# Kernel tuning notes

Hardware: AMD Instinct MI355X
Metric: run time of the kernel (lower is better)

## Reference

```python
import jax, jax.numpy as jnp
import numpy as np

N, E, C, MID = 20000, 320000, 16, 32
EPS = 1e-8

# ---- real Clebsch-Gordan (Q_J) matrices for degree pairs up to l=1, real-SH m-order (-l..l) i.e. (y,z,x) for l=1 ----

def _q_matrices():
    Q0 = np.eye(3, dtype=np.float32)[:, :, None] / np.sqrt(3.0)          # 1x1 -> J=0
    eps = np.zeros((3, 3, 3), dtype=np.float32)
    for (a, b, c_) in [(0, 1, 2), (1, 2, 0), (2, 0, 1)]:
        eps[a, b, c_] = 1.0
        eps[a, c_, b] = -1.0
    Q1 = eps / np.sqrt(2.0)                                               # 1x1 -> J=1 (cross product)
    Q2 = np.zeros((3, 3, 5), dtype=np.float32)                            # 1x1 -> J=2 (sym traceless)
    s2 = 1.0 / np.sqrt(2.0); s6 = 1.0 / np.sqrt(6.0)
    Q2[2, 0, 0] = Q2[0, 2, 0] = s2          # ~xy
    Q2[0, 1, 1] = Q2[1, 0, 1] = s2          # ~yz
    Q2[0, 0, 2] = -s6; Q2[1, 1, 2] = 2 * s6; Q2[2, 2, 2] = -s6  # ~(2z2-x2-y2)
    Q2[1, 2, 3] = Q2[2, 1, 3] = s2          # ~xz
    Q2[2, 2, 4] = s2; Q2[0, 0, 4] = -s2     # ~(x2-y2)
    return Q0, Q1, Q2

_Q0, _Q1, _Q2 = _q_matrices()


def _basis(u):
    """u: [E,3] unit edge directions -> basis tensors per (d_in,d_out) pair."""
    x, y, z = u[:, 0], u[:, 1], u[:, 2]
    Ep = u.shape[0]
    Y0 = jnp.full((Ep,), 0.28209479177387814, u.dtype)
    Y1 = 0.4886025119029199 * jnp.stack([y, z, x], -1)                    # m=-1,0,1
    Y2 = jnp.stack([1.0925484305920792 * x * y,
                    1.0925484305920792 * y * z,
                    0.31539156525252005 * (3.0 * z * z - 1.0),
                    1.0925484305920792 * x * z,
                    0.5462742152960396 * (x * x - y * y)], -1)
    b00 = Y0.reshape(Ep, 1, 1, 1, 1, 1)
    b01 = Y1.reshape(Ep, 1, 3, 1, 1, 1)
    b10 = Y1.reshape(Ep, 1, 1, 1, 3, 1)
    K0 = Y0[:, None, None] * jnp.asarray(_Q0[:, :, 0])
    K1 = jnp.einsum('em,abm->eab', Y1, jnp.asarray(_Q1))
    K2 = jnp.einsum('em,abm->eab', Y2, jnp.asarray(_Q2))
    b11 = jnp.stack([K0, K1, K2], -1).reshape(Ep, 1, 3, 1, 3, 3)          # num_freq=3 (J=0,1,2)
    return b00, b01, b10, b11


def _bn(x, g, b):  # BatchNorm1d, training-mode stats over edges, eps=1e-5
    mu = x.mean(0)
    var = ((x - mu) ** 2).mean(0)
    return (x - mu) * jax.lax.rsqrt(var + 1e-5) * g + b


def _hidden(feat, W1, b1, g1, be1, W2, b2, g2, be2):
    h = jax.nn.relu(_bn(feat @ W1 + b1, g1, be1))
    return jax.nn.relu(_bn(h @ W2 + b2, g2, be2))


def _kernel(Rflat, basis, nco, do_dim, nci, di_dim, nf):
    # RadialFunc output view: [E, nc_out, 1, nc_in, 1, num_freq]; contract freq with basis
    R = Rflat.reshape(-1, nco, 1, nci, 1, nf)
    k = (R * basis).sum(-1)                        # [E,nco,do_dim,nci,di_dim]
    return k.reshape(-1, nco * do_dim, nci * di_dim)


def _norm_bias(x, bias):  # GNormBias: relu(|x| + b) * phase
    n = jnp.sqrt((x * x).sum(-1, keepdims=True) + 1e-12)
    phase = x / jnp.maximum(n, EPS)
    return jax.nn.relu(n[..., 0] + bias)[..., None] * phase


def _forward(src, dst, pos, c, v, w,
             rW1, rb1, rg1, rbe1, rW2, rb2, rg2, rbe2,
             w3_a00, b3_a00, w3_a01, b3_a01, w3_a10, b3_a10, w3_a11, b3_a11,
             w3_b01, b3_b01, w3_b11, b3_b11,
             selfA0, selfA1, selfB1, nbias0, nbias1):
    n_nodes = c.shape[0]
    n_edges = src.shape[0]
    rel = pos[dst] - pos[src]
    r = jnp.sqrt((rel * rel).sum(-1, keepdims=True))                      # [E,1]
    u = rel / jnp.maximum(r, EPS)
    b00, b01, b10, b11 = _basis(u)
    feat = jnp.concatenate([w, r], -1)                                    # [E, edge_dim+1]
    # all 6 radial-net hiddens at once: [6,E,MID]
    H = jax.vmap(_hidden, in_axes=(None, 0, 0, 0, 0, 0, 0, 0, 0))(
        feat, rW1, rb1, rg1, rbe1, rW2, rb2, rg2, rbe2)
    deg = jax.ops.segment_sum(jnp.ones((n_edges,), feat.dtype), dst, num_segments=n_nodes)
    inv = (1.0 / jnp.maximum(deg, 1.0))[:, None, None]
    mask = (deg > 0).astype(feat.dtype)[:, None, None]
    # ---- layer A: in {0:1,1:1} -> mid {0:C,1:C} ----
    k00 = _kernel(H[0] @ w3_a00 + b3_a00, b00, C, 1, 1, 1, 1)             # [E,C,1]
    k01 = _kernel(H[1] @ w3_a01 + b3_a01, b01, C, 3, 1, 1, 1)             # [E,3C,1]
    k10 = _kernel(H[2] @ w3_a10 + b3_a10, b10, C, 1, 1, 3, 1)             # [E,C,3]
    k11 = _kernel(H[3] @ w3_a11 + b3_a11, b11, C, 3, 1, 3, 3)             # [E,3C,3]
    s0 = c[src].reshape(n_edges, 1, 1)
    s1 = v[src].reshape(n_edges, 3, 1)
    m0 = (k00 @ s0 + k10 @ s1).reshape(n_edges, C, 1)
    m1 = (k01 @ s0 + k11 @ s1).reshape(n_edges, C, 3)
    h0 = jax.ops.segment_sum(m0, dst, num_segments=n_nodes) * inv \
         + jnp.einsum('oi,nid->nod', selfA0[0], c) * mask
    h1 = jax.ops.segment_sum(m1, dst, num_segments=n_nodes) * inv \
         + jnp.einsum('oi,nid->nod', selfA1[0], v) * mask
    # ---- GNormBias on mid fiber ----
    h0 = _norm_bias(h0, nbias0)
    h1 = _norm_bias(h1, nbias1)
    # ---- layer B: mid {0:C,1:C} -> out {1:2} ----
    kb01 = _kernel(H[4] @ w3_b01 + b3_b01, b01, 2, 3, C, 1, 1)            # [E,6,C]
    kb11 = _kernel(H[5] @ w3_b11 + b3_b11, b11, 2, 3, C, 3, 3)            # [E,6,3C]
    t0 = h0[src]                                                          # [E,C,1]
    t1 = h1[src].reshape(n_edges, C * 3, 1)
    mB = (kb01 @ t0 + kb11 @ t1).reshape(n_edges, 2, 3)
    out = jax.ops.segment_sum(mB, dst, num_segments=n_nodes) * inv \
          + jnp.einsum('oi,nid->nod', selfB1[0], h1) * mask
    return out                                                            # [N,2,3]


def setup_inputs() -> dict:
    key = jax.random.key(0)
    ks = jax.random.split(key, 40)
    def rn(i, shape, scale=1.0):
        return jax.random.normal(ks[i], shape, jnp.float32) * scale
    K = 6
    sc = 1.0 / np.sqrt(MID)
    d = {}
    d['src'] = jax.random.randint(ks[0], (E,), 0, N)
    d['dst'] = jax.random.randint(ks[1], (E,), 0, N)
    d['pos'] = rn(2, (N, 3))
    d['c'] = rn(3, (N, 1, 1))
    d['v'] = rn(4, (N, 1, 3))
    d['w'] = rn(5, (E, 1))
    d['rW1'] = rn(6, (K, 2, MID), 1.0 / np.sqrt(2.0))
    d['rb1'] = jnp.zeros((K, MID), jnp.float32)
    d['rg1'] = jnp.ones((K, MID), jnp.float32)
    d['rbe1'] = jnp.zeros((K, MID), jnp.float32)
    d['rW2'] = rn(7, (K, MID, MID), sc)
    d['rb2'] = jnp.zeros((K, MID), jnp.float32)
    d['rg2'] = jnp.ones((K, MID), jnp.float32)
    d['rbe2'] = jnp.zeros((K, MID), jnp.float32)
    d['w3_a00'] = rn(8, (MID, C), sc);      d['b3_a00'] = jnp.zeros((C,), jnp.float32)
    d['w3_a01'] = rn(9, (MID, C), sc);      d['b3_a01'] = jnp.zeros((C,), jnp.float32)
    d['w3_a10'] = rn(10, (MID, C), sc);     d['b3_a10'] = jnp.zeros((C,), jnp.float32)
    d['w3_a11'] = rn(11, (MID, 3 * C), sc); d['b3_a11'] = jnp.zeros((3 * C,), jnp.float32)
    d['w3_b01'] = rn(12, (MID, 2 * C), sc); d['b3_b01'] = jnp.zeros((2 * C,), jnp.float32)
    d['w3_b11'] = rn(13, (MID, 6 * C), sc); d['b3_b11'] = jnp.zeros((6 * C,), jnp.float32)
    d['selfA0'] = rn(14, (1, C, 1))
    d['selfA1'] = rn(15, (1, C, 1))
    d['selfB1'] = rn(16, (1, 2, C), 1.0 / np.sqrt(C))
    d['nbias0'] = rn(17, (C,))
    d['nbias1'] = rn(18, (C,))
    return d


def reference(src, dst, pos, c, v, w,
              rW1, rb1, rg1, rbe1, rW2, rb2, rg2, rbe2,
              w3_a00, b3_a00, w3_a01, b3_a01, w3_a10, b3_a10, w3_a11, b3_a11,
              w3_b01, b3_b01, w3_b11, b3_b11,
              selfA0, selfA1, selfB1, nbias0, nbias1):
    return _forward(src, dst, pos, c, v, w,
                    rW1, rb1, rg1, rbe1, rW2, rb2, rg2, rbe2,
                    w3_a00, b3_a00, w3_a01, b3_a01, w3_a10, b3_a10, w3_a11, b3_a11,
                    w3_b01, b3_b01, w3_b11, b3_b11,
                    selfA0, selfA1, selfB1, nbias0, nbias1)
```

## Files before the change

### kernel.cpp

```cpp
#include <hip/hip_runtime.h>

#define NN 20000
#define NE 320000
#define CDIM 16
#define MID 32
#define EPSF 1e-8f

#define SCHED_FENCE() __builtin_amdgcn_sched_barrier(0)

#define OFF_DEGI   848
#define ZERO_WORDS 20848
#define OFF_ROWPTR 20848
#define OFF_CURSOR 40864
#define OFF_EORDER 60864
#define OFF_SRCS   380864
#define OFF_WSRT   700864
#define OFF_FW1A   1020864
#define OFF_FW1B   1021056
#define OFF_FC1    1021248
#define OFF_BN2A   1021440
#define OFF_FC2    1021632
#define OFF_FW2T   1021824
#define OFF_ECS    1027968
#define OFF_H0N    2307968
#define OFF_H1N    2627968
#define OFF_MSGA0  3587968
#define OFF_MSGA1  8707968
#define OFF_MSGB   24067968

#define Y0C   0.28209479177387814f
#define Y1C   0.4886025119029199f
#define Y2C1  1.0925484305920792f
#define Y2C2  0.31539156525252005f
#define Y2C3  0.5462742152960396f
#define S2C   0.7071067811865476f
#define S6C   0.4082482904638631f
#define K0C   0.16286750396763996f

__device__ __forceinline__ void atomAddD(double* p, double v) {
  unsafeAtomicAdd(p, v);
}

__device__ __forceinline__ void mlpH_lds(
    const float* __restrict__ a1, const float* __restrict__ b1v,
    const float* __restrict__ c1, const float* __restrict__ c2,
    const float* __restrict__ W2T, float we, float r, float* H) {
  float h[MID];
#pragma unroll
  for (int j4 = 0; j4 < 8; ++j4) {
    float4 av = ((const float4*)a1)[j4];
    float4 bv = ((const float4*)b1v)[j4];
    float4 cv = ((const float4*)c1)[j4];
    h[4 * j4 + 0] = fmaxf(fmaf(we, av.x, fmaf(r, bv.x, cv.x)), 0.0f);
    h[4 * j4 + 1] = fmaxf(fmaf(we, av.y, fmaf(r, bv.y, cv.y)), 0.0f);
    h[4 * j4 + 2] = fmaxf(fmaf(we, av.z, fmaf(r, bv.z, cv.z)), 0.0f);
    h[4 * j4 + 3] = fmaxf(fmaf(we, av.w, fmaf(r, bv.w, cv.w)), 0.0f);
  }
  SCHED_FENCE();
#pragma unroll
  for (int jg = 0; jg < 8; ++jg) {
#pragma unroll
    for (int jq = 0; jq < 4; ++jq) {
      const int j = jg * 4 + jq;
      float acc = c2[j];
      const float4* wp = (const float4*)(W2T + j * MID);
#pragma unroll
      for (int i4 = 0; i4 < 8; ++i4) {
        float4 wv = wp[i4];
        acc = fmaf(h[4 * i4 + 0], wv.x, acc);
        acc = fmaf(h[4 * i4 + 1], wv.y, acc);
        acc = fmaf(h[4 * i4 + 2], wv.z, acc);
        acc = fmaf(h[4 * i4 + 3], wv.w, acc);
      }
      H[j] = fmaxf(acc, 0.0f);
    }
    SCHED_FENCE();
  }
}

__global__ __launch_bounds__(256) void k_hist(
    const int* __restrict__ dst, float* __restrict__ ws) {
  int e = blockIdx.x * blockDim.x + threadIdx.x;
  if (e >= NE) return;
  atomicAdd((int*)ws + OFF_DEGI + dst[e], 1);
}

__global__ void k_scan(float* __restrict__ ws) {
  __shared__ int buf[256];
  __shared__ int carry;
  const int* degi = (const int*)ws + OFF_DEGI;
  int* rowptr = (int*)ws + OFF_ROWPTR;
  int* cursor = (int*)ws + OFF_CURSOR;
  int tid = threadIdx.x;
  if (tid == 0) carry = 0;
  __syncthreads();
  for (int base = 0; base < NN; base += 256) {
    int v = (base + tid < NN) ? degi[base + tid] : 0;
    buf[tid] = v;
    __syncthreads();
    for (int off = 1; off < 256; off <<= 1) {
      int t = buf[tid];
      int add = (tid >= off) ? buf[tid - off] : 0;
      __syncthreads();
      buf[tid] = t + add;
      __syncthreads();
    }
    int excl = buf[tid] - v;
    if (base + tid < NN) {
      rowptr[base + tid] = carry + excl;
      cursor[base + tid] = carry + excl;
    }
    __syncthreads();
    if (tid == 255) carry += buf[255];
    __syncthreads();
  }
  if (tid == 0) rowptr[NN] = carry;
}

__global__ __launch_bounds__(256) void k_scatter(
    const int* __restrict__ dst, float* __restrict__ ws) {
  int e = blockIdx.x * blockDim.x + threadIdx.x;
  if (e >= NE) return;
  int* cursor = (int*)ws + OFF_CURSOR;
  int* eorder = (int*)ws + OFF_EORDER;
  int d = dst[e];
  int p = atomicAdd(cursor + d, 1);
  eorder[p] = e;
}

__global__ __launch_bounds__(256) void k_geo(
    const int* __restrict__ src, const int* __restrict__ dst,
    const float* __restrict__ pos, const float* __restrict__ w,
    float* __restrict__ ws) {
  __shared__ double sred[20];
  double lw = 0, lr = 0, lww = 0, lrr = 0, lwr = 0;
  const int* eorder = (const int*)ws + OFF_EORDER;
  int* srcs = (int*)ws + OFF_SRCS;
  float* wsrt = ws + OFF_WSRT;
  float4* ecs = (float4*)(ws + OFF_ECS);
  for (int t = blockIdx.x * blockDim.x + threadIdx.x; t < NE;
       t += gridDim.x * blockDim.x) {
    int e = eorder[t];
    int s = src[e], d = dst[e];
    float dx = pos[3 * d + 0] - pos[3 * s + 0];
    float dy = pos[3 * d + 1] - pos[3 * s + 1];
    float dz = pos[3 * d + 2] - pos[3 * s + 2];
    float r = sqrtf(dx * dx + dy * dy + dz * dz);
    float ri = 1.0f / fmaxf(r, EPSF);
    ecs[t] = make_float4(r, dx * ri, dy * ri, dz * ri);
    float we = w[e];
    wsrt[t] = we;
    srcs[t] = s;
    double wd = (double)we, rd = (double)r;
    lw += wd; lr += rd; lww += wd * wd; lrr += rd * rd; lwr += wd * rd;
  }
#pragma unroll
  for (int d = 32; d >= 1; d >>= 1) {
    lw += __shfl_xor(lw, d);
    lr += __shfl_xor(lr, d);
    lww += __shfl_xor(lww, d);
    lrr += __shfl_xor(lrr, d);
    lwr += __shfl_xor(lwr, d);
  }
  int wid = threadIdx.x >> 6;
  if ((threadIdx.x & 63) == 0) {
    sred[0 * 4 + wid] = lw;
    sred[1 * 4 + wid] = lr;
    sred[2 * 4 + wid] = lww;
    sred[3 * 4 + wid] = lrr;
    sred[4 * 4 + wid] = lwr;
  }
  __syncthreads();
  if (threadIdx.x < 5) {
    double v = sred[threadIdx.x * 4 + 0] + sred[threadIdx.x * 4 + 1]
             + sred[threadIdx.x * 4 + 2] + sred[threadIdx.x * 4 + 3];
    atomAddD((double*)ws + threadIdx.x * 8, v);
  }
}

__global__ void k_fin1(const float* __restrict__ rW1, const float* __restrict__ rb1,
                       const float* __restrict__ rg1, const float* __restrict__ rbe1,
                       float* __restrict__ ws) {
  int t = threadIdx.x;
  int k = t >> 5, j = t & 31;
  const double* s1 = (const double*)ws;
  double Sw = s1[0], Sr = s1[8], Sww = s1[16], Srr = s1[24], Swr = s1[32];
  const double inv = 1.0 / (double)NE;
  double W0 = (double)rW1[k * 64 + j], W1 = (double)rW1[k * 64 + 32 + j];
  double b = (double)rb1[k * 32 + j];
  double mlin = (Sw * W0 + Sr * W1) * inv;
  double mu = mlin + b;
  double ex2 = (Sww * W0 * W0 + Srr * W1 * W1 + 2.0 * Swr * W0 * W1) * inv
             + 2.0 * b * mlin + b * b;
  double var = ex2 - mu * mu;
  double a = (double)rg1[k * 32 + j] / sqrt(var + 1e-5);
  ws[OFF_FW1A + t] = (float)(W0 * a);
  ws[OFF_FW1B + t] = (float)(W1 * a);
  ws[OFF_FC1 + t] = (float)((double)rbe1[k * 32 + j] - mlin * a);
}

__global__ __launch_bounds__(256) void k_stats2(
    const float* __restrict__ rW2, const float* __restrict__ rb2,
    float* __restrict__ ws) {
  const int k = blockIdx.y;
  const int j0 = blockIdx.z * 16;
  __shared__ __align__(16) float sW1a[32], sW1b[32], sc1[32];
  __shared__ __align__(16) float sW2c[512];
  __shared__ float sb2[16];
  __shared__ float sredf[2][16][4];
  int tid = threadIdx.x;
  if (tid < 32) {
    sW1a[tid] = ws[OFF_FW1A + k * 32 + tid];
    sW1b[tid] = ws[OFF_FW1B + k * 32 + tid];
    sc1[tid] = ws[OFF_FC1 + k * 32 + tid];
  }
  if (tid < 16) sb2[tid] = rb2[k * 32 + j0 + tid];
  for (int t = tid; t < 512; t += 256) {
    int jj = t >> 5, i = t & 31;
    sW2c[t] = rW2[k * 1024 + i * 32 + j0 + jj];
  }
  __syncthreads();
  const float4* ecs = (const float4*)(ws + OFF_ECS);
  const float* wsrt = ws + OFF_WSRT;
  float lsum[16], lsq[16];
#pragma unroll
  for (int jj = 0; jj < 16; ++jj) { lsum[jj] = 0.0f; lsq[jj] = 0.0f; }
  const int NP = NE / 2;
  for (int p = blockIdx.x * blockDim.x + tid; p < NP;
       p += gridDim.x * blockDim.x) {
    int e0 = 2 * p;
    float r0 = ecs[e0].x, r1 = ecs[e0 + 1].x;
    float w0 = wsrt[e0], w1 = wsrt[e0 + 1];
    float h0[MID], h1[MID];
#pragma unroll
    for (int j4 = 0; j4 < 8; ++j4) {
      float4 av = ((const float4*)sW1a)[j4];
      float4 bv = ((const float4*)sW1b)[j4];
      float4 cv = ((const float4*)sc1)[j4];
      h0[4 * j4 + 0] = fmaxf(fmaf(w0, av.x, fmaf(r0, bv.x, cv.x)), 0.0f);
      h1[4 * j4 + 0] = fmaxf(fmaf(w1, av.x, fmaf(r1, bv.x, cv.x)), 0.0f);
      h0[4 * j4 + 1] = fmaxf(fmaf(w0, av.y, fmaf(r0, bv.y, cv.y)), 0.0f);
      h1[4 * j4 + 1] = fmaxf(fmaf(w1, av.y, fmaf(r1, bv.y, cv.y)), 0.0f);
      h0[4 * j4 + 2] = fmaxf(fmaf(w0, av.z, fmaf(r0, bv.z, cv.z)), 0.0f);
      h1[4 * j4 + 2] = fmaxf(fmaf(w1, av.z, fmaf(r1, bv.z, cv.z)), 0.0f);
      h0[4 * j4 + 3] = fmaxf(fmaf(w0, av.w, fmaf(r0, bv.w, cv.w)), 0.0f);
      h1[4 * j4 + 3] = fmaxf(fmaf(w1, av.w, fmaf(r1, bv.w, cv.w)), 0.0f);
    }
    SCHED_FENCE();
#pragma unroll
    for (int jg = 0; jg < 4; ++jg) {
#pragma unroll
      for (int jq = 0; jq < 4; ++jq) {
        const int jj = jg * 4 + jq;
        float aE0 = sb2[jj], aE1 = sb2[jj];
        const float4* wp = (const float4*)(sW2c + jj * 32);
#pragma unroll
        for (int i4 = 0; i4 < 8; ++i4) {
          float4 wv = wp[i4];
          aE0 = fmaf(h0[4 * i4 + 0], wv.x, aE0);
          aE1 = fmaf(h1[4 * i4 + 0], wv.x, aE1);
          aE0 = fmaf(h0[4 * i4 + 1], wv.y, aE0);
          aE1 = fmaf(h1[4 * i4 + 1], wv.y, aE1);
          aE0 = fmaf(h0[4 * i4 + 2], wv.z, aE0);
          aE1 = fmaf(h1[4 * i4 + 2], wv.z, aE1);
          aE0 = fmaf(h0[4 * i4 + 3], wv.w, aE0);
          aE1 = fmaf(h1[4 * i4 + 3], wv.w, aE1);
        }
        lsum[jj] += aE0 + aE1;
        lsq[jj] = fmaf(aE0, aE0, fmaf(aE1, aE1, lsq[jj]));
      }
      SCHED_FENCE();
    }
  }
  int wid = tid >> 6;
#pragma unroll
  for (int jj = 0; jj < 16; ++jj) {
    float v1 = lsum[jj], v2 = lsq[jj];
#pragma unroll
    for (int d = 32; d >= 1; d >>= 1) {
      v1 += __shfl_xor(v1, d);
      v2 += __shfl_xor(v2, d);
    }
    if ((tid & 63) == 0) {
      sredf[0][jj][wid] = v1;
      sredf[1][jj][wid] = v2;
    }
  }
  __syncthreads();
  if (tid < 32) {
    int jj = tid & 15, which = tid >> 4;
    float v = sredf[which][jj][0] + sredf[which][jj][1]
            + sredf[which][jj][2] + sredf[which][jj][3];
    double* s2 = (double*)(ws + 80);
    atomAddD(s2 + k * 64 + which * 32 + j0 + jj, (double)v);
  }
}

__global__ void k_fin2(const float* __restrict__ rb2,
                       const float* __restrict__ rg2, const float* __restrict__ rbe2,
                       float* __restrict__ ws) {
  int t = threadIdx.x;
  int k = t >> 5, j = t & 31;
  const double* s2 = (const double*)(ws + 80);
  const double inv = 1.0 / (double)NE;
  double mu = s2[k * 64 + j] * inv;
  double ex2 = s2[k * 64 + 32 + j] * inv;
  double var = ex2 - mu * mu;
  double a = (double)rg2[t] / sqrt(var + 1e-5);
  ws[OFF_BN2A + t] = (float)a;
  ws[OFF_FC2 + t] = (float)((double)rbe2[t] + ((double)rb2[t] - mu) * a);
}

__global__ __launch_bounds__(256) void k_fold2(const float* __restrict__ rW2,
                                               float* __restrict__ ws) {
  int idx = blockIdx.x * blockDim.x + threadIdx.x;
  if (idx >= 6144) return;
  int k = idx >> 10, rem = idx & 1023;
  int j = rem >> 5, i = rem & 31;
  ws[OFF_FW2T + idx] = rW2[k * 1024 + i * 32 + j] * ws[OFF_BN2A + k * 32 + j];
}

__global__ __launch_bounds__(256) void k_passA0(
    const float* __restrict__ cI, const float* __restrict__ vI,
    const float* __restrict__ w00, const float* __restrict__ b00,
    const float* __restrict__ w10, const float* __restrict__ b10,
    float* __restrict__ ws) {
  __shared__ __align__(16) float sW1a[64], sW1b[64], sc1[64], sc2[64];
  __shared__ __align__(16) float sW2T[2048];
  __shared__ __align__(16) float sP00[512], sP10[512];
  __shared__ float sB00[16], sB10[16];
  int tid = threadIdx.x;
  if (tid < 32) {
    sW1a[tid] = ws[OFF_FW1A + tid];       sW1a[32 + tid] = ws[OFF_FW1A + 64 + tid];
    sW1b[tid] = ws[OFF_FW1B + tid];       sW1b[32 + tid] = ws[OFF_FW1B + 64 + tid];
    sc1[tid]  = ws[OFF_FC1 + tid];        sc1[32 + tid]  = ws[OFF_FC1 + 64 + tid];
    sc2[tid]  = ws[OFF_FC2 + tid];        sc2[32 + tid]  = ws[OFF_FC2 + 64 + tid];
  }
  for (int t = tid; t < 1024; t += 256) {
    sW2T[t] = ws[OFF_FW2T + t];
    sW2T[1024 + t] = ws[OFF_FW2T + 2048 + t];
  }
  for (int t = tid; t < 512; t += 256) {
    int i = t >> 4, co = t & 15;
    sP00[co * 32 + i] = w00[t];
    sP10[co * 32 + i] = w10[t];
  }
  if (tid < 16) { sB00[tid] = b00[tid]; sB10[tid] = b10[tid]; }
  __syncthreads();

  const int* srcs = (const int*)ws + OFF_SRCS;
  const float* wsrt = ws + OFF_WSRT;
  const float4* ecs = (const float4*)(ws + OFF_ECS);
  int t = blockIdx.x * blockDim.x + tid;
  if (t >= NE) return;
  int s = srcs[t];
  float4 E = ecs[t];
  float we = wsrt[t];
  float cs = cI[s];
  float v0 = vI[3 * s + 0], v1 = vI[3 * s + 1], v2 = vI[3 * s + 2];
  float dY1v = Y1C * (E.z * v0 + E.w * v1 + E.y * v2);

  float H[MID], m0[CDIM];
  mlpH_lds(sW1a, sW1b, sc1, sc2, sW2T, we, E.x, H);
  float f0 = Y0C * cs;
#pragma unroll
  for (int cg = 0; cg < 4; ++cg) {
#pragma unroll
    for (int cq = 0; cq < 4; ++cq) {
      const int co = cg * 4 + cq;
      float a = sB00[co];
      const float4* wp = (const float4*)(sP00 + co * 32);
#pragma unroll
      for (int i4 = 0; i4 < 8; ++i4) {
        float4 wv = wp[i4];
        a = fmaf(H[4 * i4 + 0], wv.x, a);
        a = fmaf(H[4 * i4 + 1], wv.y, a);
        a = fmaf(H[4 * i4 + 2], wv.z, a);
        a = fmaf(H[4 * i4 + 3], wv.w, a);
      }
      m0[co] = a * f0;
    }
    SCHED_FENCE();
  }
  mlpH_lds(sW1a + 32, sW1b + 32, sc1 + 32, sc2 + 32, sW2T + 1024, we, E.x, H);
#pragma unroll
  for (int cg = 0; cg < 4; ++cg) {
#pragma unroll
    for (int cq = 0; cq < 4; ++cq) {
      const int co = cg * 4 + cq;
      float a = sB10[co];
      const float4* wp = (const float4*)(sP10 + co * 32);
#pragma unroll
      for (int i4 = 0; i4 < 8; ++i4) {
        float4 wv = wp[i4];
        a = fmaf(H[4 * i4 + 0], wv.x, a);
        a = fmaf(H[4 * i4 + 1], wv.y, a);
        a = fmaf(H[4 * i4 + 2], wv.z, a);
        a = fmaf(H[4 * i4 + 3], wv.w, a);
      }
      m0[co] = fmaf(a, dY1v, m0[co]);
    }
    SCHED_FENCE();
  }
  float4* mp = (float4*)(ws + OFF_MSGA0) + t * 4;
#pragma unroll
  for (int q = 0; q < 4; ++q)
    mp[q] = make_float4(m0[4 * q], m0[4 * q + 1], m0[4 * q + 2], m0[4 * q + 3]);
}

__global__ __launch_bounds__(256) void k_passA1(
    const float* __restrict__ cI, const float* __restrict__ vI,
    const float* __restrict__ w01, const float* __restrict__ b01,
    const float* __restrict__ w11, const float* __restrict__ b11,
    float* __restrict__ ws) {
  __shared__ __align__(16) float sW1a[64], sW1b[64], sc1[64], sc2[64];
  __shared__ __align__(16) float sW2T[2048];
  __shared__ __align__(16) float sP01[512], sP11[1536];
  __shared__ float sB01[16], sB11[48];
  int tid = threadIdx.x;
  if (tid < 32) {
    sW1a[tid] = ws[OFF_FW1A + 32 + tid];  sW1a[32 + tid] = ws[OFF_FW1A + 96 + tid];
    sW1b[tid] = ws[OFF_FW1B + 32 + tid];  sW1b[32 + tid] = ws[OFF_FW1B + 96 + tid];
    sc1[tid]  = ws[OFF_FC1 + 32 + tid];   sc1[32 + tid]  = ws[OFF_FC1 + 96 + tid];
    sc2[tid]  = ws[OFF_FC2 + 32 + tid];   sc2[32 + tid]  = ws[OFF_FC2 + 96 + tid];
  }
  for (int t = tid; t < 1024; t += 256) {
    sW2T[t] = ws[OFF_FW2T + 1024 + t];
    sW2T[1024 + t] = ws[OFF_FW2T + 3072 + t];
  }
  for (int t = tid; t < 512; t += 256) {
    int i = t >> 4, co = t & 15;
    sP01[co * 32 + i] = w01[t];
  }
  for (int t = tid; t < 1536; t += 256) {
    int i = t / 48, c = t - i * 48;
    sP11[c * 32 + i] = w11[t];
  }
  if (tid < 16) sB01[tid] = b01[tid];
  if (tid < 48) sB11[tid] = b11[tid];
  __syncthreads();

  const int* srcs = (const int*)ws + OFF_SRCS;
  const float* wsrt = ws + OFF_WSRT;
  const float4* ecs = (const float4*)(ws + OFF_ECS);
  int t = blockIdx.x * blockDim.x + tid;
  if (t >= NE) return;
  int s = srcs[t];
  float4 E = ecs[t];
  float we = wsrt[t];
  float cs = cI[s];

  float H[MID];
  float ra[16];
  mlpH_lds(sW1a, sW1b, sc1, sc2, sW2T, we, E.x, H);
#pragma unroll
  for (int cg = 0; cg < 4; ++cg) {
#pragma unroll
    for (int cq = 0; cq < 4; ++cq) {
      const int co = cg * 4 + cq;
      float a = sB01[co];
      const float4* wp = (const float4*)(sP01 + co * 32);
#pragma unroll
      for (int i4 = 0; i4 < 8; ++i4) {
        float4 wv = wp[i4];
        a = fmaf(H[4 * i4 + 0], wv.x, a);
        a = fmaf(H[4 * i4 + 1], wv.y, a);
        a = fmaf(H[4 * i4 + 2], wv.z, a);
        a = fmaf(H[4 * i4 + 3], wv.w, a);
      }
      ra[co] = a;
    }
    SCHED_FENCE();
  }
  mlpH_lds(sW1a + 32, sW1b + 32, sc1 + 32, sc2 + 32, sW2T + 1024, we, E.x, H);
  float y10 = Y1C * E.z, y11 = Y1C * E.w, y12 = Y1C * E.y;
  float KV[3][3];
  {
    float ux = E.y, uy = E.z, uz = E.w;
    float y20 = Y2C1 * ux * uy, y21 = Y2C1 * uy * uz;
    float y22 = Y2C2 * (3.0f * uz * uz - 1.0f);
    float y23 = Y2C1 * ux * uz, y24 = Y2C3 * (ux * ux - uy * uy);
    float S00 = -S6C * y22 - S2C * y24;
    float S11 = 2.0f * S6C * y22;
    float S22 = -S6C * y22 + S2C * y24;
    float S01 = S2C * y21, S02 = S2C * y20, S12 = S2C * y23;
    float v0 = vI[3 * s + 0], v1 = vI[3 * s + 1], v2 = vI[3 * s + 2];
    KV[0][0] = K0C * v0; KV[0][1] = K0C * v1; KV[0][2] = K0C * v2;
    KV[1][0] = S2C * (y12 * v1 - y11 * v2);
    KV[1][1] = S2C * (y10 * v2 - y12 * v0);
    KV[1][2] = S2C * (y11 * v0 - y10 * v1);
    KV[2][0] = S00 * v0 + S01 * v1 + S02 * v2;
    KV[2][1] = S01 * v0 + S11 * v1 + S12 * v2;
    KV[2][2] = S02 * v0 + S12 * v1 + S22 * v2;
  }
  float cy0 = cs * y10, cy1 = cs * y11, cy2 = cs * y12;
#pragma unroll 1
  for (int g = 0; g < 4; ++g) {
    float a[12];
#pragma unroll
    for (int q = 0; q < 4; ++q) {
      int co = g * 4 + q;
      float R0 = sB11[co * 3 + 0], R1 = sB11[co * 3 + 1], R2 = sB11[co * 3 + 2];
      const float4* p0 = (const float4*)(sP11 + (co * 3 + 0) * 32);
      const float4* p1 = (const float4*)(sP11 + (co * 3 + 1) * 32);
      const float4* p2 = (const float4*)(sP11 + (co * 3 + 2) * 32);
#pragma unroll
      for (int i4 = 0; i4 < 8; ++i4) {
        float4 w0v = p0[i4], w1v = p1[i4], w2v = p2[i4];
        float h0 = H[4 * i4 + 0], h1 = H[4 * i4 + 1];
        float h2 = H[4 * i4 + 2], h3 = H[4 * i4 + 3];
        R0 = fmaf(h0, w0v.x, R0); R1 = fmaf(h0, w1v.x, R1); R2 = fmaf(h0, w2v.x, R2);
        R0 = fmaf(h1, w0v.y, R0); R1 = fmaf(h1, w1v.y, R1); R2 = fmaf(h1, w2v.y, R2);
        R0 = fmaf(h2, w0v.z, R0); R1 = fmaf(h2, w1v.z, R1); R2 = fmaf(h2, w2v.z, R2);
        R0 = fmaf(h3, w0v.w, R0); R1 = fmaf(h3, w1v.w, R1); R2 = fmaf(h3, w2v.w, R2);
      }
      float r_ = ra[co];
      a[q * 3 + 0] = fmaf(r_, cy0, R0 * KV[0][0] + R1 * KV[1][0] + R2 * KV[2][0]);
      a[q * 3 + 1] = fmaf(r_, cy1, R0 * KV[0][1] + R1 * KV[1][1] + R2 * KV[2][1]);
      a[q * 3 + 2] = fmaf(r_, cy2, R0 * KV[0][2] + R1 * KV[1][2] + R2 * KV[2][2]);
    }
    float4* mp = (float4*)(ws + OFF_MSGA1 + g * (NE * 12)) + t * 3;
    mp[0] = make_float4(a[0], a[1], a[2], a[3]);
    mp[1] = make_float4(a[4], a[5], a[6], a[7]);
    mp[2] = make_float4(a[8], a[9], a[10], a[11]);
    SCHED_FENCE();
  }
}

__global__ __launch_bounds__(256) void k_nodeA(
    const float* __restrict__ cI, const float* __restrict__ vI,
    const float* __restrict__ selfA0, const float* __restrict__ selfA1,
    const float* __restrict__ nbias0, const float* __restrict__ nbias1,
    float* __restrict__ ws) {
  int idx = blockIdx.x * blockDim.x + threadIdx.x;
  if (idx >= NN * CDIM) return;
  int n = idx >> 4, co = idx & 15;
  const int* rowptr = (const int*)ws + OFF_ROWPTR;
  int r0 = rowptr[n], r1 = rowptr[n + 1];
  const float* mA0 = ws + OFF_MSGA0;
  const float* mA1 = ws + OFF_MSGA1 + (co >> 2) * (NE * 12) + (co & 3) * 3;
  float x0 = 0.0f, xa = 0.0f, xb = 0.0f, xc = 0.0f;
  for (int row = r0; row < r1; ++row) {
    x0 += mA0[row * 16 + co];
    xa += mA1[row * 12 + 0];
    xb += mA1[row * 12 + 1];
    xc += mA1[row * 12 + 2];
  }
  float dg = (float)(r1 - r0);
  float iv = 1.0f / fmaxf(dg, 1.0f);
  float mk = dg > 0.0f ? 1.0f : 0.0f;
  x0 = x0 * iv + selfA0[co] * cI[n] * mk;
  float n0 = sqrtf(x0 * x0 + 1e-12f);
  ws[OFF_H0N + idx] = fmaxf(n0 + nbias0[co], 0.0f) * (x0 / fmaxf(n0, EPSF));
  xa = xa * iv + selfA1[co] * vI[3 * n + 0] * mk;
  xb = xb * iv + selfA1[co] * vI[3 * n + 1] * mk;
  xc = xc * iv + selfA1[co] * vI[3 * n + 2] * mk;
  float nv = sqrtf(xa * xa + xb * xb + xc * xc + 1e-12f);
  float sc = fmaxf(nv + nbias1[co], 0.0f) / fmaxf(nv, EPSF);
  ws[OFF_H1N + idx * 3 + 0] = xa * sc;
  ws[OFF_H1N + idx * 3 + 1] = xb * sc;
  ws[OFF_H1N + idx * 3 + 2] = xc * sc;
}

__global__ __launch_bounds__(256) void k_passB(
    const float* __restrict__ wb01, const float* __restrict__ bb01,
    const float* __restrict__ wb11, const float* __restrict__ bb11,
    float* __restrict__ ws) {
  __shared__ __align__(16) float sW1a[64], sW1b[64], sc1[64], sc2[64];
  __shared__ __align__(16) float sW2T[2048];
  __shared__ __align__(16) float sPB01[1024];
  __shared__ __align__(16) float sPB11[3072];
  __shared__ float sBB01[32];
  __shared__ float sBB11[96];
  int tid = threadIdx.x;
  if (tid < 64) {
    sW1a[tid] = ws[OFF_FW1A + 128 + tid];
    sW1b[tid] = ws[OFF_FW1B + 128 + tid];
    sc1[tid] = ws[OFF_FC1 + 128 + tid];
    sc2[tid] = ws[OFF_FC2 + 128 + tid];
  }
  for (int t = tid; t < 2048; t += 256) sW2T[t] = ws[OFF_FW2T + 4096 + t];
  for (int t = tid; t < 1024; t += 256) {
    int i = t >> 5, c = t & 31;
    int o = c >> 4, ci = c & 15;
    sPB01[(ci * 2 + o) * 32 + i] = wb01[t];
  }
  for (int t = tid; t < 3072; t += 256) {
    int i = t / 96, c = t - i * 96;
    int o = c / 48, rem = c - o * 48;
    int ci = rem / 3, f = rem - ci * 3;
    sPB11[(ci * 6 + o * 3 + f) * 32 + i] = wb11[t];
  }
  if (tid < 32) {
    int o = tid >> 4, ci = tid & 15;
    sBB01[ci * 2 + o] = bb01[tid];
  }
  if (tid < 96) {
    int o = tid / 48, rem = tid - o * 48;
    int ci = rem / 3, f = rem - ci * 3;
    sBB11[ci * 6 + o * 3 + f] = bb11[tid];
  }
  __syncthreads();

  const int* srcs = (const int*)ws + OFF_SRCS;
  const float* wsrt = ws + OFF_WSRT;
  const float4* ecs = (const float4*)(ws + OFF_ECS);
  int t = blockIdx.x * blockDim.x + tid;
  if (t >= NE) return;
  int s = srcs[t];
  float4 E = ecs[t];
  float we = wsrt[t];

  float H[MID];
  mlpH_lds(sW1a, sW1b, sc1, sc2, sW2T, we, E.x, H);
  const float* h0p = ws + OFF_H0N + s * CDIM;
  float A0 = 0.0f, A1 = 0.0f;
#pragma unroll 1
  for (int ci = 0; ci < CDIM; ++ci) {
    float b = h0p[ci];
    float R0 = sBB01[ci * 2 + 0], R1 = sBB01[ci * 2 + 1];
    const float4* p0 = (const float4*)(sPB01 + (ci * 2 + 0) * 32);
    const float4* p1 = (const float4*)(sPB01 + (ci * 2 + 1) * 32);
#pragma unroll
    for (int i4 = 0; i4 < 8; ++i4) {
      float4 w0v = p0[i4], w1v = p1[i4];
      float h0 = H[4 * i4 + 0], h1 = H[4 * i4 + 1];
      float h2 = H[4 * i4 + 2], h3 = H[4 * i4 + 3];
      R0 = fmaf(h0, w0v.x, R0); R1 = fmaf(h0, w1v.x, R1);
      R0 = fmaf(h1, w0v.y, R0); R1 = fmaf(h1, w1v.y, R1);
      R0 = fmaf(h2, w0v.z, R0); R1 = fmaf(h2, w1v.z, R1);
      R0 = fmaf(h3, w0v.w, R0); R1 = fmaf(h3, w1v.w, R1);
    }
    A0 = fmaf(R0, b, A0);
    A1 = fmaf(R1, b, A1);
    SCHED_FENCE();
  }
  mlpH_lds(sW1a + 32, sW1b + 32, sc1 + 32, sc2 + 32, sW2T + 1024, we, E.x, H);
  const float* h1p = ws + OFF_H1N + s * CDIM * 3;
  float G[6][3];
#pragma unroll
  for (int of = 0; of < 6; ++of) {
    G[of][0] = 0.0f; G[of][1] = 0.0f; G[of][2] = 0.0f;
  }
#pragma unroll 1
  for (int ci = 0; ci < CDIM; ++ci) {
    float b0 = h1p[ci * 3 + 0], b1 = h1p[ci * 3 + 1], b2 = h1p[ci * 3 + 2];
#pragma unroll
    for (int of = 0; of < 6; ++of) {
      float R = sBB11[ci * 6 + of];
      const float4* wp = (const float4*)(sPB11 + (ci * 6 + of) * 32);
#pragma unroll
      for (int i4 = 0; i4 < 8; ++i4) {
        float4 wv = wp[i4];
        R = fmaf(H[4 * i4 + 0], wv.x, R);
        R = fmaf(H[4 * i4 + 1], wv.y, R);
        R = fmaf(H[4 * i4 + 2], wv.z, R);
        R = fmaf(H[4 * i4 + 3], wv.w, R);
      }
      G[of][0] = fmaf(R, b0, G[of][0]);
      G[of][1] = fmaf(R, b1, G[of][1]);
      G[of][2] = fmaf(R, b2, G[of][2]);
    }
    SCHED_FENCE();
  }
  {
    float ux = E.y, uy = E.z, uz = E.w;
    float y10 = Y1C * uy, y11 = Y1C * uz, y12 = Y1C * ux;
    float y20 = Y2C1 * ux * uy, y21 = Y2C1 * uy * uz;
    float y22 = Y2C2 * (3.0f * uz * uz - 1.0f);
    float y23 = Y2C1 * ux * uz, y24 = Y2C3 * (ux * ux - uy * uy);
    float S00 = -S6C * y22 - S2C * y24;
    float S11 = 2.0f * S6C * y22;
    float S22 = -S6C * y22 + S2C * y24;
    float S01 = S2C * y21, S02 = S2C * y20, S12 = S2C * y23;
    float4* mp = (float4*)(ws + OFF_MSGB) + t * 2;
#pragma unroll
    for (int o = 0; o < 2; ++o) {
      float Ao = (o == 0) ? A0 : A1;
      float m0 = Ao * y10 + K0C * G[o * 3 + 0][0]
               + S2C * (y12 * G[o * 3 + 1][1] - y11 * G[o * 3 + 1][2])
               + S00 * G[o * 3 + 2][0] + S01 * G[o * 3 + 2][1] + S02 * G[o * 3 + 2][2];
      float m1 = Ao * y11 + K0C * G[o * 3 + 0][1]
               + S2C * (y10 * G[o * 3 + 1][2] - y12 * G[o * 3 + 1][0])
               + S01 * G[o * 3 + 2][0] + S11 * G[o * 3 + 2][1] + S12 * G[o * 3 + 2][2];
      float m2 = Ao * y12 + K0C * G[o * 3 + 0][2]
               + S2C * (y11 * G[o * 3 + 1][0] - y10 * G[o * 3 + 1][1])
               + S02 * G[o * 3 + 2][0] + S12 * G[o * 3 + 2][1] + S22 * G[o * 3 + 2][2];
      mp[o] = make_float4(m0, m1, m2, 0.0f);
    }
  }
}

__global__ __launch_bounds__(256) void k_nodeB(
    const float* __restrict__ selfB1, float* __restrict__ out,
    const float* __restrict__ ws) {
  int idx = blockIdx.x * blockDim.x + threadIdx.x;
  if (idx >= NN * 6) return;
  int n = idx / 6;
  int q = idx - n * 6;
  int o = q / 3, a = q - o * 3;
  const int* rowptr = (const int*)ws + OFF_ROWPTR;
  int r0 = rowptr[n], r1 = rowptr[n + 1];
  const float* msgB = ws + OFF_MSGB;
  int col = o * 4 + a;
  float sum = 0.0f;
  for (int row = r0; row < r1; ++row) sum += msgB[row * 8 + col];
  float dg = (float)(r1 - r0);
  float iv = 1.0f / fmaxf(dg, 1.0f);
  float mk = dg > 0.0f ? 1.0f : 0.0f;
  const float* h1p = ws + OFF_H1N + n * CDIM * 3;
  float self = 0.0f;
#pragma unroll
  for (int ci = 0; ci < CDIM; ++ci)
    self = fmaf(selfB1[o * CDIM + ci], h1p[ci * 3 + a], self);
  out[idx] = sum * iv + self * mk;
}

extern "C" void kernel_launch(void* const* d_in, const int* in_sizes, int n_in,
                              void* d_out, int out_size, void* d_ws, size_t ws_size,
                              hipStream_t stream) {
  (void)in_sizes; (void)n_in; (void)out_size; (void)ws_size;
  const int* src = (const int*)d_in[0];
  const int* dst = (const int*)d_in[1];
  const float* pos = (const float*)d_in[2];
  const float* cI = (const float*)d_in[3];
  const float* vI = (const float*)d_in[4];
  const float* w = (const float*)d_in[5];
  const float* rW1 = (const float*)d_in[6];
  const float* rb1 = (const float*)d_in[7];
  const float* rg1 = (const float*)d_in[8];
  const float* rbe1 = (const float*)d_in[9];
  const float* rW2 = (const float*)d_in[10];
  const float* rb2 = (const float*)d_in[11];
  const float* rg2 = (const float*)d_in[12];
  const float* rbe2 = (const float*)d_in[13];
  const float* w3_a00 = (const float*)d_in[14];
  const float* b3_a00 = (const float*)d_in[15];
  const float* w3_a01 = (const float*)d_in[16];
  const float* b3_a01 = (const float*)d_in[17];
  const float* w3_a10 = (const float*)d_in[18];
  const float* b3_a10 = (const float*)d_in[19];
  const float* w3_a11 = (const float*)d_in[20];
  const float* b3_a11 = (const float*)d_in[21];
  const float* w3_b01 = (const float*)d_in[22];
  const float* b3_b01 = (const float*)d_in[23];
  const float* w3_b11 = (const float*)d_in[24];
  const float* b3_b11 = (const float*)d_in[25];
  const float* selfA0 = (const float*)d_in[26];
  const float* selfA1 = (const float*)d_in[27];
  const float* selfB1 = (const float*)d_in[28];
  const float* nbias0 = (const float*)d_in[29];
  const float* nbias1 = (const float*)d_in[30];
  float* ws = (float*)d_ws;
  float* out = (float*)d_out;

  hipMemsetAsync(d_ws, 0, (size_t)ZERO_WORDS * 4, stream);

  k_hist<<<1250, 256, 0, stream>>>(dst, ws);
  k_scan<<<1, 256, 0, stream>>>(ws);
  k_scatter<<<1250, 256, 0, stream>>>(dst, ws);
  k_geo<<<1250, 256, 0, stream>>>(src, dst, pos, w, ws);
  k_fin1<<<1, 192, 0, stream>>>(rW1, rb1, rg1, rbe1, ws);
  k_stats2<<<dim3(256, 6, 2), 256, 0, stream>>>(rW2, rb2, ws);
  k_fin2<<<1, 192, 0, stream>>>(rb2, rg2, rbe2, ws);
  k_fold2<<<24, 256, 0, stream>>>(rW2, ws);
  k_passA0<<<1250, 256, 0, stream>>>(cI, vI, w3_a00, b3_a00, w3_a10, b3_a10, ws);
  k_passA1<<<1250, 256, 0, stream>>>(cI, vI, w3_a01, b3_a01, w3_a11, b3_a11, ws);
  k_nodeA<<<1250, 256, 0, stream>>>(cI, vI, selfA0, selfA1, nbias0, nbias1, ws);
  k_passB<<<1250, 256, 0, stream>>>(w3_b01, b3_b01, w3_b11, b3_b11, ws);
  k_nodeB<<<469, 256, 0, stream>>>(selfB1, out, ws);
}
```

Baseline: 546.3 us.

## Process two edges per thread in passB to reuse LDS weight reads

k_passB now has each thread handle an adjacent pair of edges. It uses a new two-edge MLP helper and interleaved FMA chains, so every LDS weight float4 load feeds two edges' accumulators. The block size drops to 128 and the grid stays at 1250, so the total thread count is half the edge count. The aim is to halve LDS bandwidth per edge and raise ILP, at the cost of roughly doubled register use and possibly lower occupancy. passA0's sW2T fill loop is also reshaped into a single equivalent loop.

```diff
diff --git a/kernel.cpp b/kernel.cpp
--- a/kernel.cpp
+++ b/kernel.cpp
@@ -73,6 +73,55 @@
         acc = fmaf(h[4 * i4 + 3], wv.w, acc);
       }
       H[j] = fmaxf(acc, 0.0f);
+    }
+    SCHED_FENCE();
+  }
+}
+
+__device__ __forceinline__ void mlpH2_lds(
+    const float* __restrict__ a1, const float* __restrict__ b1v,
+    const float* __restrict__ c1, const float* __restrict__ c2,
+    const float* __restrict__ W2T,
+    float weA, float rA, float weB, float rB,
+    float* HA, float* HB) {
+  float hA[MID], hB[MID];
+#pragma unroll
+  for (int j4 = 0; j4 < 8; ++j4) {
+    float4 av = ((const float4*)a1)[j4];
+    float4 bv = ((const float4*)b1v)[j4];
+    float4 cv = ((const float4*)c1)[j4];
+    hA[4 * j4 + 0] = fmaxf(fmaf(weA, av.x, fmaf(rA, bv.x, cv.x)), 0.0f);
+    hB[4 * j4 + 0] = fmaxf(fmaf(weB, av.x, fmaf(rB, bv.x, cv.x)), 0.0f);
+    hA[4 * j4 + 1] = fmaxf(fmaf(weA, av.y, fmaf(rA, bv.y, cv.y)), 0.0f);
+    hB[4 * j4 + 1] = fmaxf(fmaf(weB, av.y, fmaf(rB, bv.y, cv.y)), 0.0f);
+    hA[4 * j4 + 2] = fmaxf(fmaf(weA, av.z, fmaf(rA, bv.z, cv.z)), 0.0f);
+    hB[4 * j4 + 2] = fmaxf(fmaf(weB, av.z, fmaf(rB, bv.z, cv.z)), 0.0f);
+    hA[4 * j4 + 3] = fmaxf(fmaf(weA, av.w, fmaf(rA, bv.w, cv.w)), 0.0f);
+    hB[4 * j4 + 3] = fmaxf(fmaf(weB, av.w, fmaf(rB, bv.w, cv.w)), 0.0f);
+  }
+  SCHED_FENCE();
+#pragma unroll
+  for (int jg = 0; jg < 8; ++jg) {
+#pragma unroll
+    for (int jq = 0; jq < 4; ++jq) {
+      const int j = jg * 4 + jq;
+      float c2v = c2[j];
+      float accA = c2v, accB = c2v;
+      const float4* wp = (const float4*)(W2T + j * MID);
+#pragma unroll
+      for (int i4 = 0; i4 < 8; ++i4) {
+        float4 wv = wp[i4];
+        accA = fmaf(hA[4 * i4 + 0], wv.x, accA);
+        accB = fmaf(hB[4 * i4 + 0], wv.x, accB);
+        accA = fmaf(hA[4 * i4 + 1], wv.y, accA);
+        accB = fmaf(hB[4 * i4 + 1], wv.y, accB);
+        accA = fmaf(hA[4 * i4 + 2], wv.z, accA);
+        accB = fmaf(hB[4 * i4 + 2], wv.z, accB);
+        accA = fmaf(hA[4 * i4 + 3], wv.w, accA);
+        accB = fmaf(hB[4 * i4 + 3], wv.w, accB);
+      }
+      HA[j] = fmaxf(accA, 0.0f);
+      HB[j] = fmaxf(accB, 0.0f);
     }
     SCHED_FENCE();
   }
@@ -336,9 +385,8 @@
     sc1[tid]  = ws[OFF_FC1 + tid];        sc1[32 + tid]  = ws[OFF_FC1 + 64 + tid];
     sc2[tid]  = ws[OFF_FC2 + tid];        sc2[32 + tid]  = ws[OFF_FC2 + 64 + tid];
   }
-  for (int t = tid; t < 1024; t += 256) {
-    sW2T[t] = ws[OFF_FW2T + t];
-    sW2T[1024 + t] = ws[OFF_FW2T + 2048 + t];
+  for (int t = tid; t < 2048; t += 256) {
+    sW2T[t] = ws[OFF_FW2T + ((t < 1024) ? t : (1024 + t))];
   }
   for (int t = tid; t < 512; t += 256) {
     int i = t >> 4, co = t & 15;
@@ -562,7 +610,7 @@
   ws[OFF_H1N + idx * 3 + 2] = xc * sc;
 }
 
-__global__ __launch_bounds__(256) void k_passB(
+__global__ __launch_bounds__(128) void k_passB(
     const float* __restrict__ wb01, const float* __restrict__ bb01,
     const float* __restrict__ wb11, const float* __restrict__ bb11,
     float* __restrict__ ws) {
@@ -579,13 +627,13 @@
     sc1[tid] = ws[OFF_FC1 + 128 + tid];
     sc2[tid] = ws[OFF_FC2 + 128 + tid];
   }
-  for (int t = tid; t < 2048; t += 256) sW2T[t] = ws[OFF_FW2T + 4096 + t];
-  for (int t = tid; t < 1024; t += 256) {
+  for (int t = tid; t < 2048; t += 128) sW2T[t] = ws[OFF_FW2T + 4096 + t];
+  for (int t = tid; t < 1024; t += 128) {
     int i = t >> 5, c = t & 31;
     int o = c >> 4, ci = c & 15;
     sPB01[(ci * 2 + o) * 32 + i] = wb01[t];
   }
-  for (int t = tid; t < 3072; t += 256) {
+  for (int t = tid; t < 3072; t += 128) {
     int i = t / 96, c = t - i * 96;
     int o = c / 48, rem = c - o * 48;
     int ci = rem / 3, f = rem - ci * 3;
@@ -605,88 +653,138 @@
   const int* srcs = (const int*)ws + OFF_SRCS;
   const float* wsrt = ws + OFF_WSRT;
   const float4* ecs = (const float4*)(ws + OFF_ECS);
-  int t = blockIdx.x * blockDim.x + tid;
-  if (t >= NE) return;
-  int s = srcs[t];
-  float4 E = ecs[t];
-  float we = wsrt[t];
-
-  float H[MID];
-  mlpH_lds(sW1a, sW1b, sc1, sc2, sW2T, we, E.x, H);
-  const float* h0p = ws + OFF_H0N + s * CDIM;
-  float A0 = 0.0f, A1 = 0.0f;
+  const int NP = NE / 2;
+  int p = blockIdx.x * blockDim.x + tid;
+  if (p >= NP) return;
+  {
+    int tA = 2 * p, tB = 2 * p + 1;
+    int sA = srcs[tA], sB_ = srcs[tB];
+    float4 EA = ecs[tA], EB = ecs[tB];
+    float weA = wsrt[tA], weB = wsrt[tB];
+
+    float HA[MID], HB[MID];
+    mlpH2_lds(sW1a, sW1b, sc1, sc2, sW2T, weA, EA.x, weB, EB.x, HA, HB);
+    const float* h0pA = ws + OFF_H0N + sA * CDIM;
+    const float* h0pB = ws + OFF_H0N + sB_ * CDIM;
+    float A0A = 0.0f, A1A = 0.0f, A0B = 0.0f, A1B = 0.0f;
 #pragma unroll 1
-  for (int ci = 0; ci < CDIM; ++ci) {
-    float b = h0p[ci];
-    float R0 = sBB01[ci * 2 + 0], R1 = sBB01[ci * 2 + 1];
-    const float4* p0 = (const float4*)(sPB01 + (ci * 2 + 0) * 32);
-    const float4* p1 = (const float4*)(sPB01 + (ci * 2 + 1) * 32);
-#pragma unroll
-    for (int i4 = 0; i4 < 8; ++i4) {
-      float4 w0v = p0[i4], w1v = p1[i4];
-      float h0 = H[4 * i4 + 0], h1 = H[4 * i4 + 1];
-      float h2 = H[4 * i4 + 2], h3 = H[4 * i4 + 3];
-      R0 = fmaf(h0, w0v.x, R0); R1 = fmaf(h0, w1v.x, R1);
-      R0 = fmaf(h1, w0v.y, R0); R1 = fmaf(h1, w1v.y, R1);
-      R0 = fmaf(h2, w0v.z, R0); R1 = fmaf(h2, w1v.z, R1);
-      R0 = fmaf(h3, w0v.w, R0); R1 = fmaf(h3, w1v.w, R1);
-    }
-    A0 = fmaf(R0, b, A0);
-    A1 = fmaf(R1, b, A1);
-    SCHED_FENCE();
-  }
-  mlpH_lds(sW1a + 32, sW1b + 32, sc1 + 32, sc2 + 32, sW2T + 1024, we, E.x, H);
-  const float* h1p = ws + OFF_H1N + s * CDIM * 3;
-  float G[6][3];
-#pragma unroll
-  for (int of = 0; of < 6; ++of) {
-    G[of][0] = 0.0f; G[of][1] = 0.0f; G[of][2] = 0.0f;
-  }
+    for (int ci = 0; ci < CDIM; ++ci) {
+      float bA = h0pA[ci], bB = h0pB[ci];
+      float R0A = sBB01[ci * 2 + 0], R1A = sBB01[ci * 2 + 1];
+      float R0B = R0A, R1B = R1A;
+      const float4* p0 = (const float4*)(sPB01 + (ci * 2 + 0) * 32);
+      const float4* p1 = (const float4*)(sPB01 + (ci * 2 + 1) * 32);
+#pragma unroll
+      for (int i4 = 0; i4 < 8; ++i4) {
+        float4 w0v = p0[i4], w1v = p1[i4];
+        float hA0 = HA[4 * i4 + 0], hB0 = HB[4 * i4 + 0];
+        float hA1 = HA[4 * i4 + 1], hB1 = HB[4 * i4 + 1];
+        float hA2 = HA[4 * i4 + 2], hB2 = HB[4 * i4 + 2];
+        float hA3 = HA[4 * i4 + 3], hB3 = HB[4 * i4 + 3];
+        R0A = fmaf(hA0, w0v.x, R0A); R0B = fmaf(hB0, w0v.x, R0B);
+        R1A = fmaf(hA0, w1v.x, R1A); R1B = fmaf(hB0, w1v.x, R1B);
+        R0A = fmaf(hA1, w0v.y, R0A); R0B = fmaf(hB1, w0v.y, R0B);
+        R1A = fmaf(hA1, w1v.y, R1A); R1B = fmaf(hB1, w1v.y, R1B);
+        R0A = fmaf(hA2, w0v.z, R0A); R0B = fmaf(hB2, w0v.z, R0B);
+        R1A = fmaf(hA2, w1v.z, R1A); R1B = fmaf(hB2, w1v.z, R1B);
+        R0A = fmaf(hA3, w0v.w, R0A); R0B = fmaf(hB3, w0v.w, R0B);
+        R1A = fmaf(hA3, w1v.w, R1A); R1B = fmaf(hB3, w1v.w, R1B);
+      }
+      A0A = fmaf(R0A, bA, A0A); A1A = fmaf(R1A, bA, A1A);
+      A0B = fmaf(R0B, bB, A0B); A1B = fmaf(R1B, bB, A1B);
+      SCHED_FENCE();
+    }
+    mlpH2_lds(sW1a + 32, sW1b + 32, sc1 + 32, sc2 + 32, sW2T + 1024,
+              weA, EA.x, weB, EB.x, HA, HB);
+    const float* h1pA = ws + OFF_H1N + sA * CDIM * 3;
+    const float* h1pB = ws + OFF_H1N + sB_ * CDIM * 3;
+    float GA[6][3], GB[6][3];
+#pragma unroll
+    for (int of = 0; of < 6; ++of) {
+      GA[of][0] = 0.0f; GA[of][1] = 0.0f; GA[of][2] = 0.0f;
+      GB[of][0] = 0.0f; GB[of][1] = 0.0f; GB[of][2] = 0.0f;
+    }
 #pragma unroll 1
-  for (int ci = 0; ci < CDIM; ++ci) {
-    float b0 = h1p[ci * 3 + 0], b1 = h1p[ci * 3 + 1], b2 = h1p[ci * 3 + 2];
-#pragma unroll
-    for (int of = 0; of < 6; ++of) {
-      float R = sBB11[ci * 6 + of];
-      const float4* wp = (const float4*)(sPB11 + (ci * 6 + of) * 32);
-#pragma unroll
-      for (int i4 = 0; i4 < 8; ++i4) {
-        float4 wv = wp[i4];
-        R = fmaf(H[4 * i4 + 0], wv.x, R);
-        R = fmaf(H[4 * i4 + 1], wv.y, R);
-        R = fmaf(H[4 * i4 + 2], wv.z, R);
-        R = fmaf(H[4 * i4 + 3], wv.w, R);
-      }
-      G[of][0] = fmaf(R, b0, G[of][0]);
-      G[of][1] = fmaf(R, b1, G[of][1]);
-      G[of][2] = fmaf(R, b2, G[of][2]);
-    }
-    SCHED_FENCE();
-  }
-  {
-    float ux = E.y, uy = E.z, uz = E.w;
-    float y10 = Y1C * uy, y11 = Y1C * uz, y12 = Y1C * ux;
-    float y20 = Y2C1 * ux * uy, y21 = Y2C1 * uy * uz;
-    float y22 = Y2C2 * (3.0f * uz * uz - 1.0f);
-    float y23 = Y2C1 * ux * uz, y24 = Y2C3 * (ux * ux - uy * uy);
-    float S00 = -S6C * y22 - S2C * y24;
-    float S11 = 2.0f * S6C * y22;
-    float S22 = -S6C * y22 + S2C * y24;
-    float S01 = S2C * y21, S02 = S2C * y20, S12 = S2C * y23;
-    float4* mp = (float4*)(ws + OFF_MSGB) + t * 2;
-#pragma unroll
-    for (int o = 0; o < 2; ++o) {
-      float Ao = (o == 0) ? A0 : A1;
-      float m0 = Ao * y10 + K0C * G[o * 3 + 0][0]
-               + S2C * (y12 * G[o * 3 + 1][1] - y11 * G[o * 3 + 1][2])
-               + S00 * G[o * 3 + 2][0] + S01 * G[o * 3 + 2][1] + S02 * G[o * 3 + 2][2];
-      float m1 = Ao * y11 + K0C * G[o * 3 + 0][1]
-               + S2C * (y10 * G[o * 3 + 1][2] - y12 * G[o * 3 + 1][0])
-               + S01 * G[o * 3 + 2][0] + S11 * G[o * 3 + 2][1] + S12 * G[o * 3 + 2][2];
-      float m2 = Ao * y12 + K0C * G[o * 3 + 0][2]
-               + S2C * (y11 * G[o * 3 + 1][0] - y10 * G[o * 3 + 1][1])
-               + S02 * G[o * 3 + 2][0] + S12 * G[o * 3 + 2][1] + S22 * G[o * 3 + 2][2];
-      mp[o] = make_float4(m0, m1, m2, 0.0f);
+    for (int ci = 0; ci < CDIM; ++ci) {
+      float bA0 = h1pA[ci * 3 + 0], bA1 = h1pA[ci * 3 + 1], bA2 = h1pA[ci * 3 + 2];
+      float bB0 = h1pB[ci * 3 + 0], bB1 = h1pB[ci * 3 + 1], bB2 = h1pB[ci * 3 + 2];
+#pragma unroll
+      for (int of = 0; of < 6; ++of) {
+        float RA = sBB11[ci * 6 + of];
+        float RB = RA;
+        const float4* wp = (const float4*)(sPB11 + (ci * 6 + of) * 32);
+#pragma unroll
+        for (int i4 = 0; i4 < 8; ++i4) {
+          float4 wv = wp[i4];
+          RA = fmaf(HA[4 * i4 + 0], wv.x, RA);
+          RB = fmaf(HB[4 * i4 + 0], wv.x, RB);
+          RA = fmaf(HA[4 * i4 + 1], wv.y, RA);
+          RB = fmaf(HB[4 * i4 + 1], wv.y, RB);
+          RA = fmaf(HA[4 * i4 + 2], wv.z, RA);
+          RB = fmaf(HB[4 * i4 + 2], wv.z, RB);
+          RA = fmaf(HA[4 * i4 + 3], wv.w, RA);
+          RB = fmaf(HB[4 * i4 + 3], wv.w, RB);
+        }
+        GA[of][0] = fmaf(RA, bA0, GA[of][0]);
+        GA[of][1] = fmaf(RA, bA1, GA[of][1]);
+        GA[of][2] = fmaf(RA, bA2, GA[of][2]);
+        GB[of][0] = fmaf(RB, bB0, GB[of][0]);
+        GB[of][1] = fmaf(RB, bB1, GB[of][1]);
+        GB[of][2] = fmaf(RB, bB2, GB[of][2]);
+      }
+      SCHED_FENCE();
+    }
+    {
+      float ux = EA.y, uy = EA.z, uz = EA.w;
+      float y10 = Y1C * uy, y11 = Y1C * uz, y12 = Y1C * ux;
+      float y20 = Y2C1 * ux * uy, y21 = Y2C1 * uy * uz;
+      float y22 = Y2C2 * (3.0f * uz * uz - 1.0f);
+      float y23 = Y2C1 * ux * uz, y24 = Y2C3 * (ux * ux - uy * uy);
+      float S00 = -S6C * y22 - S2C * y24;
+      float S11 = 2.0f * S6C * y22;
+      float S22 = -S6C * y22 + S2C * y24;
+      float S01 = S2C * y21, S02 = S2C * y20, S12 = S2C * y23;
+      float4* mp = (float4*)(ws + OFF_MSGB) + tA * 2;
+#pragma unroll
+      for (int o = 0; o < 2; ++o) {
+        float Ao = (o == 0) ? A0A : A1A;
+        float m0 = Ao * y10 + K0C * GA[o * 3 + 0][0]
+                 + S2C * (y12 * GA[o * 3 + 1][1] - y11 * GA[o * 3 + 1][2])
+                 + S00 * GA[o * 3 + 2][0] + S01 * GA[o * 3 + 2][1] + S02 * GA[o * 3 + 2][2];
+        float m1 = Ao * y11 + K0C * GA[o * 3 + 0][1]
+                 + S2C * (y10 * GA[o * 3 + 1][2] - y12 * GA[o * 3 + 1][0])
+                 + S01 * GA[o * 3 + 2][0] + S11 * GA[o * 3 + 2][1] + S12 * GA[o * 3 + 2][2];
+        float m2 = Ao * y12 + K0C * GA[o * 3 + 0][2]
+                 + S2C * (y11 * GA[o * 3 + 1][0] - y10 * GA[o * 3 + 1][1])
+                 + S02 * GA[o * 3 + 2][0] + S12 * GA[o * 3 + 2][1] + S22 * GA[o * 3 + 2][2];
+        mp[o] = make_float4(m0, m1, m2, 0.0f);
+      }
+    }
+    {
+      float ux = EB.y, uy = EB.z, uz = EB.w;
+      float y10 = Y1C * uy, y11 = Y1C * uz, y12 = Y1C * ux;
+      float y20 = Y2C1 * ux * uy, y21 = Y2C1 * uy * uz;
+      float y22 = Y2C2 * (3.0f * uz * uz - 1.0f);
+      float y23 = Y2C1 * ux * uz, y24 = Y2C3 * (ux * ux - uy * uy);
+      float S00 = -S6C * y22 - S2C * y24;
+      float S11 = 2.0f * S6C * y22;
+      float S22 = -S6C * y22 + S2C * y24;
+      float S01 = S2C * y21, S02 = S2C * y20, S12 = S2C * y23;
+      float4* mp = (float4*)(ws + OFF_MSGB) + tB * 2;
+#pragma unroll
+      for (int o = 0; o < 2; ++o) {
+        float Ao = (o == 0) ? A0B : A1B;
+        float m0 = Ao * y10 + K0C * GB[o * 3 + 0][0]
+                 + S2C * (y12 * GB[o * 3 + 1][1] - y11 * GB[o * 3 + 1][2])
+                 + S00 * GB[o * 3 + 2][0] + S01 * GB[o * 3 + 2][1] + S02 * GB[o * 3 + 2][2];
+        float m1 = Ao * y11 + K0C * GB[o * 3 + 0][1]
+                 + S2C * (y10 * GB[o * 3 + 1][2] - y12 * GB[o * 3 + 1][0])
+                 + S01 * GB[o * 3 + 2][0] + S11 * GB[o * 3 + 2][1] + S12 * GB[o * 3 + 2][2];
+        float m2 = Ao * y12 + K0C * GB[o * 3 + 0][2]
+                 + S2C * (y11 * GB[o * 3 + 1][0] - y10 * GB[o * 3 + 1][1])
+                 + S02 * GB[o * 3 + 2][0] + S12 * GB[o * 3 + 2][1] + S22 * GB[o * 3 + 2][2];
+        mp[o] = make_float4(m0, m1, m2, 0.0f);
+      }
     }
   }
 }
@@ -767,6 +865,6 @@
   k_passA0<<<1250, 256, 0, stream>>>(cI, vI, w3_a00, b3_a00, w3_a10, b3_a10, ws);
   k_passA1<<<1250, 256, 0, stream>>>(cI, vI, w3_a01, b3_a01, w3_a11, b3_a11, ws);
   k_nodeA<<<1250, 256, 0, stream>>>(cI, vI, selfA0, selfA1, nbias0, nbias1, ws);
-  k_passB<<<1250, 256, 0, stream>>>(w3_b01, b3_b01, w3_b11, b3_b11, ws);
+  k_passB<<<1250, 128, 0, stream>>>(w3_b01, b3_b01, w3_b11, b3_b11, ws);
   k_nodeB<<<469, 256, 0, stream>>>(selfB1, out, ws);
 }
```

Result: no change. 545.7 us (-0.1%).
